# Optimization experiments

Measured on AMD Instinct MI355X. Metric: run time of the kernel, lower is better.

## Reference

```python
import jax, jax.numpy as jnp
import numpy as np

N, M, E = 400000, 100000, 3200000
C_FEAT = 61            # per-point feature channels
D_IN = 64              # 3 (rel xyz) + C_FEAT
D0, D1, D2 = 64, 128, 256  # mlp = [64, 128, 256]
EPS = 1e-5


def setup_inputs() -> dict:
    key = jax.random.key(0)
    ks = jax.random.split(key, 16)
    inp = {}
    inp['point_bxyz'] = jax.random.uniform(ks[0], (N, 4), dtype=jnp.float32) * 50.0
    inp['point_feat'] = jax.random.normal(ks[1], (N, C_FEAT), dtype=jnp.float32)
    inp['sample_idx'] = jax.random.randint(ks[2], (M,), 0, N)
    inp['e_point'] = jax.random.randint(ks[3], (E,), 0, N)
    inp['e_new'] = jnp.sort(jax.random.randint(ks[4], (E,), 0, M))
    # PointConv: Linear(D_IN -> D0)
    inp['W0'] = jax.random.normal(ks[5], (D_IN, D0), dtype=jnp.float32) / np.sqrt(D_IN)
    inp['b0'] = jnp.zeros((D0,), dtype=jnp.float32)
    # mlp_convs[0]: Linear(D0 -> D1) + BN
    inp['W1'] = jax.random.normal(ks[6], (D0, D1), dtype=jnp.float32) / np.sqrt(D0)
    inp['b1'] = jnp.zeros((D1,), dtype=jnp.float32)
    inp['g1'] = jnp.ones((D1,), dtype=jnp.float32)
    inp['beta1'] = jnp.zeros((D1,), dtype=jnp.float32)
    # mlp_convs[1]: Linear(D1 -> D2) + BN
    inp['W2'] = jax.random.normal(ks[7], (D1, D2), dtype=jnp.float32) / np.sqrt(D1)
    inp['b2'] = jnp.zeros((D2,), dtype=jnp.float32)
    inp['g2'] = jnp.ones((D2,), dtype=jnp.float32)
    inp['beta2'] = jnp.zeros((D2,), dtype=jnp.float32)
    return inp


def _bn_relu(x, g, b):
    # BatchNorm1d in training mode: batch stats, biased variance
    mu = x.mean(axis=0)
    var = x.var(axis=0)
    return jax.nn.relu((x - mu) * jax.lax.rsqrt(var + EPS) * g + b)


def reference(point_bxyz, point_feat, sample_idx, e_point, e_new,
              W0, b0, W1, b1, g1, beta1, W2, b2, g2, beta2):
    num_new = sample_idx.shape[0]
    new_bxyz = point_bxyz[sample_idx]                      # [M, 4]
    # PointConv: per-edge relative position encoding + feature gather
    rel = point_bxyz[e_point, 1:4] - new_bxyz[e_new, 1:4]  # [E, 3]
    edge_in = jnp.concatenate([rel, point_feat[e_point]], axis=-1)  # [E, D_IN]
    h = jax.nn.relu(edge_in @ W0 + b0)                     # [E, D0]
    # per-neighborhood max aggregation (scatter-max), empty segments -> 0
    agg = jax.ops.segment_max(h, e_new, num_segments=num_new)
    agg = jnp.where(jnp.isneginf(agg), 0.0, agg)           # [M, D0]
    # trailing Linear + BN + ReLU stack
    x = _bn_relu(agg @ W1 + b1, g1, beta1)                 # [M, D1]
    x = _bn_relu(x @ W2 + b2, g2, beta2)                   # [M, D2]
    return new_bxyz, x
```

## Files before the change

### kernel.cpp

```cpp
#include <hip/hip_runtime.h>

#define EPS 1e-5f
#define ECHUNK 64

typedef _Float16 half8 __attribute__((ext_vector_type(8)));
typedef _Float16 half4v __attribute__((ext_vector_type(4)));
typedef float float4v __attribute__((ext_vector_type(4)));

static __device__ __forceinline__ unsigned pkmax16(unsigned a, unsigned b) {
    unsigned d;
    asm("v_pk_max_f16 %0, %1, %2" : "=v"(d) : "v"(a), "v"(b));
    return d;
}

__global__ void gather_kernel(const float4* __restrict__ bxyz, const int* __restrict__ sidx,
                              float4* __restrict__ out, int M) {
    int i = blockIdx.x * blockDim.x + threadIdx.x;
    if (i < M) out[i] = bxyz[sidx[i]];
}

__global__ void prep_kernel(const float* __restrict__ W0, const float* __restrict__ W1,
                            const float* __restrict__ W2, _Float16* __restrict__ W0t,
                            _Float16* __restrict__ W1t, _Float16* __restrict__ W2t) {
    int i = blockIdx.x * blockDim.x + threadIdx.x;
    if (i < 4096) {
        int k = i >> 6, n = i & 63;
        W0t[(size_t)n * 64 + k] = (_Float16)W0[i];
    } else if (i < 12288) {
        int j = i - 4096; int k = j >> 7, n = j & 127;
        W1t[(size_t)n * 64 + k] = (_Float16)W1[j];
    } else if (i < 45056) {
        int j = i - 12288; int k = j >> 8, n = j & 255;
        W2t[(size_t)n * 128 + k] = (_Float16)W2[j];
    }
}

__global__ __launch_bounds__(256, 4) void point_kernel(
    const float* __restrict__ feat, const float4* __restrict__ bxyz4,
    const _Float16* __restrict__ W0t, const float* __restrict__ b0,
    _Float16* __restrict__ GDh, int N) {
    __shared__ _Float16 As[128 * 72];
    int t = threadIdx.x;
    int row0 = blockIdx.x * 128;
    if (t < 128) {
        int r = min(row0 + t, N - 1);
        float4 P = bxyz4[r];
        As[t * 72 + 0] = (_Float16)P.y;
        As[t * 72 + 1] = (_Float16)P.z;
        As[t * 72 + 2] = (_Float16)P.w;
    }
    const float* fbase = feat + (size_t)row0 * 61;
    int avail = (int)min((size_t)7808, (size_t)(N - row0) * 61);
#pragma unroll
    for (int j = 0; j < 8; ++j) {
        int base = (t + j * 256) * 4;
        if (base < avail) {
            float4 v = *(const float4*)&fbase[base];
            float fv[4] = {v.x, v.y, v.z, v.w};
#pragma unroll
            for (int u = 0; u < 4; ++u) {
                int flat = base + u;
                int r = flat / 61;
                int k = flat - r * 61;
                As[r * 72 + 3 + k] = (_Float16)fv[u];
            }
        }
    }
    __syncthreads();
    int w = t >> 6, lane = t & 63, quad = lane >> 4, l16 = lane & 15;
    int mwave = w * 32;
    float4v acc[2][4] = {};
#pragma unroll
    for (int kc = 0; kc < 2; ++kc) {
        int koff = kc * 32 + quad * 8;
        half8 af[2], bf[4];
#pragma unroll
        for (int mt = 0; mt < 2; ++mt)
            af[mt] = *(const half8*)&As[(mwave + mt * 16 + l16) * 72 + koff];
#pragma unroll
        for (int nt = 0; nt < 4; ++nt)
            bf[nt] = *(const half8*)&W0t[(size_t)(nt * 16 + l16) * 64 + koff];
#pragma unroll
        for (int mt = 0; mt < 2; ++mt)
#pragma unroll
            for (int nt = 0; nt < 4; ++nt)
                acc[mt][nt] = __builtin_amdgcn_mfma_f32_16x16x32_f16(af[mt], bf[nt], acc[mt][nt], 0, 0, 0);
    }
    float b0v[4];
#pragma unroll
    for (int nt = 0; nt < 4; ++nt) b0v[nt] = b0[nt * 16 + l16];
    __syncthreads();
#pragma unroll
    for (int mt = 0; mt < 2; ++mt)
#pragma unroll
        for (int i = 0; i < 4; ++i) {
            int rloc = mwave + mt * 16 + quad * 4 + i;
#pragma unroll
            for (int nt = 0; nt < 4; ++nt)
                As[rloc * 72 + nt * 16 + l16] = (_Float16)(acc[mt][nt][i] + b0v[nt]);
        }
    __syncthreads();
#pragma unroll
    for (int j = 0; j < 4; ++j) {
        int i8 = t + j * 256;
        int r = i8 >> 3, c8 = i8 & 7;
        if (row0 + r < N)
            *(half8*)&GDh[(size_t)(row0 + r) * 64 + c8 * 8] = *(const half8*)&As[r * 72 + c8 * 8];
    }
}

__global__ __launch_bounds__(256, 8) void edge_kernel(
    const float4* __restrict__ nbxyz4,
    const int* __restrict__ e_point, const int* __restrict__ e_new,
    const _Float16* __restrict__ GDh, const float* __restrict__ W0,
    float* __restrict__ agg, int E) {
    int lane = threadIdx.x & 63;
    int gwave = blockIdx.x * 4 + (threadIdx.x >> 6);
    int base = __builtin_amdgcn_readfirstlane(gwave * ECHUNK);
    if (base >= E) return;
    int n = min(ECHUNK, E - base);

    if (n == ECHUNK) {
        bool hi = lane >= 32;
        int c0 = lane & 31;
        int ch = c0 * 2 + (hi ? 1 : 0);
        float wx = W0[ch], wy = W0[64 + ch], wz = W0[128 + ch];
        const unsigned NEGP = 0xFBFFFBFFu;

        int ep = e_point[base + lane];
        int en = e_new[base + lane];

        int prev = __shfl_up(en, 1);
        unsigned long long bm = __ballot(lane == 0 || en != prev);
        unsigned blo = __builtin_amdgcn_readfirstlane((unsigned)bm);
        unsigned bhi = __builtin_amdgcn_readfirstlane((unsigned)(bm >> 32));
        unsigned long long bmask = (((unsigned long long)bhi << 32) | blo) & ~1ull;

        int curseg = __builtin_amdgcn_readlane(en, 0);
        unsigned amax = NEGP;
        int laneoff = c0 * 4;
        int permbase = hi ? 4 : 0;

#define FLUSH_SEG()  do {                                                          \
        unsigned other_ = (unsigned)__shfl_xor((int)amax, 32);                     \
        unsigned comb_ = pkmax16(amax, other_);                                    \
        unsigned bits_ = hi ? (comb_ >> 16) : (comb_ & 0xffffu);                   \
        _Float16 hm_ = __builtin_bit_cast(_Float16, (unsigned short)bits_);        \
        float4 Q_ = nbxyz4[curseg];                                                \
        float S_ = fmaf(Q_.y, wx, fmaf(Q_.z, wy, Q_.w * wz));                      \
        float v_ = fmaxf(0.f, (float)hm_ - S_);                                    \
        atomicMax((int*)&agg[(size_t)curseg * 64 + ch], __float_as_int(v_));       \
    } while (0)

#pragma unroll
        for (int grp = 0; grp < 2; ++grp) {
            unsigned gu[16];
#pragma unroll
            for (int j = 0; j < 16; ++j) {
                int p = __builtin_amdgcn_ds_bpermute(permbase + (grp * 16 + j) * 8, ep);
                unsigned off = ((unsigned)p << 7) + laneoff;
                gu[j] = *(const unsigned*)((const char*)GDh + off);
            }
#pragma unroll
            for (int j = 0; j < 16; ++j) {
                int e0 = (grp * 16 + j) * 2;
                if ((bmask >> e0) & 1) {
                    FLUSH_SEG();
                    curseg = __builtin_amdgcn_readlane(en, e0);
                    amax = NEGP;
                }
                if ((bmask >> (e0 + 1)) & 1) {
                    amax = pkmax16(amax, hi ? NEGP : gu[j]);
                    FLUSH_SEG();
                    curseg = __builtin_amdgcn_readlane(en, e0 + 1);
                    amax = hi ? gu[j] : NEGP;
                } else {
                    amax = pkmax16(amax, gu[j]);
                }
            }
        }
        FLUSH_SEG();
#undef FLUSH_SEG
    } else {
        float wx = W0[lane], wy = W0[64 + lane], wz = W0[128 + lane];
        int idx = min(base + lane, E - 1);
        int ep = e_point[idx];
        int en = e_new[idx];
        int curseg = -1;
        float runmax = 0.f, S = 0.f;
        for (int e = 0; e < n; ++e) {
            int p = __builtin_amdgcn_readlane(ep, e);
            int s = __builtin_amdgcn_readlane(en, e);
            if (s != curseg) {
                if (curseg >= 0)
                    atomicMax((int*)&agg[(size_t)curseg * 64 + lane], __float_as_int(runmax));
                curseg = s;
                runmax = 0.f;
                float4 Q = nbxyz4[s];
                S = fmaf(Q.y, wx, fmaf(Q.z, wy, Q.w * wz));
            }
            float h = (float)GDh[(size_t)p * 64 + lane] - S;
            runmax = fmaxf(runmax, h);
        }
        if (curseg >= 0)
            atomicMax((int*)&agg[(size_t)curseg * 64 + lane], __float_as_int(runmax));
    }
}

__global__ __launch_bounds__(256, 2) void gemm1_kernel(
    const float* __restrict__ agg, const _Float16* __restrict__ W1t,
    _Float16* __restrict__ y1h, float* __restrict__ p1sum, float* __restrict__ p1sq, int M) {
    __shared__ _Float16 As[128 * 72];
    __shared__ float red[4096];
    int t = threadIdx.x;
    int row0 = blockIdx.x * 128;
#pragma unroll
    for (int j = 0; j < 8; ++j) {
        int i4 = t + j * 256;
        int r = i4 >> 4, k4 = i4 & 15;
        float4 v = make_float4(0.f, 0.f, 0.f, 0.f);
        if (row0 + r < M) v = ((const float4*)agg)[(size_t)(row0 + r) * 16 + k4];
        half4v h;
        h[0] = (_Float16)v.x; h[1] = (_Float16)v.y; h[2] = (_Float16)v.z; h[3] = (_Float16)v.w;
        *(half4v*)&As[r * 72 + k4 * 4] = h;
    }
    __syncthreads();
    int w = t >> 6, lane = t & 63, quad = lane >> 4, l16 = lane & 15;
    int mwave = w * 32;
    float4v acc[2][8] = {};
#pragma unroll
    for (int kc = 0; kc < 2; ++kc) {
        int koff = kc * 32 + quad * 8;
        half8 af[2], bf[8];
#pragma unroll
        for (int mt = 0; mt < 2; ++mt)
            af[mt] = *(const half8*)&As[(mwave + mt * 16 + l16) * 72 + koff];
#pragma unroll
        for (int nt = 0; nt < 8; ++nt)
            bf[nt] = *(const half8*)&W1t[(size_t)(nt * 16 + l16) * 64 + koff];
#pragma unroll
        for (int mt = 0; mt < 2; ++mt)
#pragma unroll
            for (int nt = 0; nt < 8; ++nt)
                acc[mt][nt] = __builtin_amdgcn_mfma_f32_16x16x32_f16(af[mt], bf[nt], acc[mt][nt], 0, 0, 0);
    }
    float s[8] = {}, q[8] = {};
#pragma unroll
    for (int mt = 0; mt < 2; ++mt)
#pragma unroll
        for (int i = 0; i < 4; ++i)
#pragma unroll
            for (int nt = 0; nt < 8; ++nt) {
                float a = acc[mt][nt][i];
                s[nt] += a; q[nt] += a * a;
            }
    int slot = w * 4 + quad;
#pragma unroll
    for (int nt = 0; nt < 8; ++nt) {
        int c = nt * 16 + l16;
        red[c * 16 + slot] = s[nt];
        red[2048 + c * 16 + slot] = q[nt];
    }
    __syncthreads();
    if (t < 128) {
        float ss = 0.f, qq = 0.f;
#pragma unroll
        for (int i = 0; i < 16; ++i) { ss += red[t * 16 + i]; qq += red[2048 + t * 16 + i]; }
        p1sum[(size_t)blockIdx.x * 128 + t] = ss;
        p1sq[(size_t)blockIdx.x * 128 + t] = qq;
    }
#pragma unroll
    for (int half = 0; half < 2; ++half) {
#pragma unroll
        for (int mt = 0; mt < 2; ++mt)
#pragma unroll
            for (int i = 0; i < 4; ++i) {
                int rloc = mwave + mt * 16 + quad * 4 + i;
#pragma unroll
                for (int nt = 0; nt < 4; ++nt)
                    As[rloc * 72 + nt * 16 + l16] = (_Float16)acc[mt][half * 4 + nt][i];
            }
        __syncthreads();
#pragma unroll
        for (int j = 0; j < 4; ++j) {
            int i8 = t + j * 256;
            int r = i8 >> 3, c8 = i8 & 7;
            if (row0 + r < M)
                *(half8*)&y1h[(size_t)(row0 + r) * 128 + half * 64 + c8 * 8] =
                    *(const half8*)&As[r * 72 + c8 * 8];
        }
        __syncthreads();
    }
}

__global__ void stats_kernel(const float* __restrict__ psum, const float* __restrict__ psq,
                             const float* __restrict__ g, const float* __restrict__ beta,
                             float* __restrict__ scale, float* __restrict__ shift,
                             int nblk, int ncols, float invM) {
    __shared__ float ss[256], qq[256];
    int c = blockIdx.x;
    int t = threadIdx.x;
    float s = 0.f, q = 0.f;
    for (int b = t; b < nblk; b += 256) {
        s += psum[(size_t)b * ncols + c];
        q += psq[(size_t)b * ncols + c];
    }
    ss[t] = s; qq[t] = q;
    __syncthreads();
    for (int off = 128; off > 0; off >>= 1) {
        if (t < off) { ss[t] += ss[t + off]; qq[t] += qq[t + off]; }
        __syncthreads();
    }
    if (t == 0) {
        float mean = ss[0] * invM;
        float var = qq[0] * invM - mean * mean;
        float sc = g[c] * rsqrtf(var + EPS);
        scale[c] = sc;
        shift[c] = beta[c] - mean * sc;
    }
}

__global__ __launch_bounds__(256, 2) void gemm2_kernel(
    const _Float16* __restrict__ y1h, const _Float16* __restrict__ W2t,
    const float* __restrict__ scale1, const float* __restrict__ shift1,
    float* __restrict__ yout, float* __restrict__ p2sum, float* __restrict__ p2sq,
    int M, int nbn) {
    __shared__ _Float16 As[128 * 136];
    __shared__ _Float16 Bs[128 * 136];
    int t = threadIdx.x;
    int bm = blockIdx.x / nbn;
    int bn = blockIdx.x % nbn;
    int row0 = bm * 128;
#pragma unroll
    for (int j = 0; j < 8; ++j) {
        int i8 = t + j * 256;
        int r = i8 >> 4, k8 = i8 & 15;
        half8 hv = {};
        if (row0 + r < M) {
            half8 y = *(const half8*)&y1h[(size_t)(row0 + r) * 128 + k8 * 8];
            float4 sca = ((const float4*)scale1)[k8 * 2];
            float4 scb = ((const float4*)scale1)[k8 * 2 + 1];
            float4 sha = ((const float4*)shift1)[k8 * 2];
            float4 shb = ((const float4*)shift1)[k8 * 2 + 1];
            float sc[8] = {sca.x, sca.y, sca.z, sca.w, scb.x, scb.y, scb.z, scb.w};
            float sh[8] = {sha.x, sha.y, sha.z, sha.w, shb.x, shb.y, shb.z, shb.w};
#pragma unroll
            for (int u = 0; u < 8; ++u)
                hv[u] = (_Float16)fmaxf(0.f, fmaf((float)y[u], sc[u], sh[u]));
        }
        *(half8*)&As[r * 136 + k8 * 8] = hv;
    }
    int n0 = bn * 128;
#pragma unroll
    for (int j = 0; j < 8; ++j) {
        int i8 = t + j * 256;
        int nn = i8 >> 4, k8 = i8 & 15;
        *(half8*)&Bs[nn * 136 + k8 * 8] = *(const half8*)&W2t[(size_t)(n0 + nn) * 128 + k8 * 8];
    }
    __syncthreads();
    int w = t >> 6, lane = t & 63;
    int quad = lane >> 4, l16 = lane & 15;
    int mwave = (w >> 1) * 64, nwave = (w & 1) * 64;
    float4v acc[4][4] = {};
#pragma unroll
    for (int kc = 0; kc < 4; ++kc) {
        int koff = kc * 32 + quad * 8;
        half8 af[4], bf[4];
#pragma unroll
        for (int mt = 0; mt < 4; ++mt)
            af[mt] = *(const half8*)&As[(mwave + mt * 16 + l16) * 136 + koff];
#pragma unroll
        for (int nt = 0; nt < 4; ++nt)
            bf[nt] = *(const half8*)&Bs[(nwave + nt * 16 + l16) * 136 + koff];
#pragma unroll
        for (int mt = 0; mt < 4; ++mt)
#pragma unroll
            for (int nt = 0; nt < 4; ++nt)
                acc[mt][nt] = __builtin_amdgcn_mfma_f32_16x16x32_f16(af[mt], bf[nt], acc[mt][nt], 0, 0, 0);
    }
    float s[4] = {}, q[4] = {};
    int colbase = n0 + nwave + l16;
#pragma unroll
    for (int mt = 0; mt < 4; ++mt) {
#pragma unroll
        for (int i = 0; i < 4; ++i) {
            int row = row0 + mwave + mt * 16 + quad * 4 + i;
            if (row < M) {
#pragma unroll
                for (int nt = 0; nt < 4; ++nt)
                    yout[(size_t)row * 256 + colbase + nt * 16] = acc[mt][nt][i];
            }
#pragma unroll
            for (int nt = 0; nt < 4; ++nt) {
                float a = acc[mt][nt][i];
                s[nt] += a; q[nt] += a * a;
            }
        }
    }
    __syncthreads();
    float* red = (float*)As;
    int slot = (w >> 1) * 4 + quad;
#pragma unroll
    for (int nt = 0; nt < 4; ++nt) {
        int c = (w & 1) * 64 + nt * 16 + l16;
        red[c * 8 + slot] = s[nt];
        red[1024 + c * 8 + slot] = q[nt];
    }
    __syncthreads();
    if (t < 128) {
        float ss = 0.f, qq = 0.f;
#pragma unroll
        for (int i = 0; i < 8; ++i) { ss += red[t * 8 + i]; qq += red[1024 + t * 8 + i]; }
        p2sum[(size_t)bm * 256 + n0 + t] = ss;
        p2sq[(size_t)bm * 256 + n0 + t] = qq;
    }
}

__global__ void apply2_kernel(float4* __restrict__ x, const float* __restrict__ scale2,
                              const float* __restrict__ shift2, int n4) {
    int i = blockIdx.x * blockDim.x + threadIdx.x;
    if (i >= n4) return;
    int c4 = i & 63;
    float4 v = x[i];
    float4 sc = ((const float4*)scale2)[c4];
    float4 sh = ((const float4*)shift2)[c4];
    v.x = fmaxf(0.f, fmaf(v.x, sc.x, sh.x));
    v.y = fmaxf(0.f, fmaf(v.y, sc.y, sh.y));
    v.z = fmaxf(0.f, fmaf(v.z, sc.z, sh.z));
    v.w = fmaxf(0.f, fmaf(v.w, sc.w, sh.w));
    x[i] = v;
}

extern "C" void kernel_launch(void* const* d_in, const int* in_sizes, int n_in,
                              void* d_out, int out_size, void* d_ws, size_t ws_size,
                              hipStream_t stream) {
    const float* bxyz  = (const float*)d_in[0];
    const float* feat  = (const float*)d_in[1];
    const int*   sidx  = (const int*)d_in[2];
    const int*   e_point = (const int*)d_in[3];
    const int*   e_new = (const int*)d_in[4];
    const float* W0    = (const float*)d_in[5];
    const float* b0    = (const float*)d_in[6];
    const float* W1    = (const float*)d_in[7];
    const float* g1    = (const float*)d_in[9];
    const float* beta1 = (const float*)d_in[10];
    const float* W2    = (const float*)d_in[11];
    const float* g2    = (const float*)d_in[13];
    const float* beta2 = (const float*)d_in[14];
    int N = in_sizes[0] / 4;
    int M = in_sizes[2];
    int E = in_sizes[3];

    float* out0 = (float*)d_out;
    float* out1 = (float*)d_out + (size_t)M * 4;

    float* ws = (float*)d_ws;
    size_t o = 0;
    float* agg = ws + o; o += (size_t)M * 64;
    _Float16* y1h = (_Float16*)(ws + o); o += (size_t)M * 64;
    _Float16* GDh = (_Float16*)(ws + o); o += (size_t)N * 32;
    _Float16* W0t = (_Float16*)(ws + o); o += 2048;
    _Float16* W1t = (_Float16*)(ws + o); o += 4096;
    _Float16* W2t = (_Float16*)(ws + o); o += 16384;
    int nblk1 = (M + 127) / 128;
    int nblk2m = (M + 127) / 128;
    int nbn = 2;
    float* p1sum = ws + o; o += (size_t)nblk1 * 128;
    float* p1sq  = ws + o; o += (size_t)nblk1 * 128;
    float* p2sum = ws + o; o += (size_t)nblk2m * 256;
    float* p2sq  = ws + o; o += (size_t)nblk2m * 256;
    float* scale1 = ws + o; o += 128;
    float* shift1 = ws + o; o += 128;
    float* scale2 = ws + o; o += 256;
    float* shift2 = ws + o; o += 256;

    hipMemsetAsync(agg, 0, (size_t)M * 64 * sizeof(float), stream);
    gather_kernel<<<(M + 255) / 256, 256, 0, stream>>>((const float4*)bxyz, sidx, (float4*)out0, M);
    prep_kernel<<<176, 256, 0, stream>>>(W0, W1, W2, W0t, W1t, W2t);
    point_kernel<<<(N + 127) / 128, 256, 0, stream>>>(feat, (const float4*)bxyz, W0t, b0, GDh, N);
    int nwaves = (E + ECHUNK - 1) / ECHUNK;
    edge_kernel<<<(nwaves + 3) / 4, 256, 0, stream>>>((const float4*)out0, e_point, e_new,
                                                      GDh, W0, agg, E);
    gemm1_kernel<<<nblk1, 256, 0, stream>>>(agg, W1t, y1h, p1sum, p1sq, M);
    stats_kernel<<<128, 256, 0, stream>>>(p1sum, p1sq, g1, beta1, scale1, shift1, nblk1, 128, 1.f / M);
    gemm2_kernel<<<nblk2m * nbn, 256, 0, stream>>>(y1h, W2t, scale1, shift1, out1, p2sum, p2sq, M, nbn);
    stats_kernel<<<256, 256, 0, stream>>>(p2sum, p2sq, g2, beta2, scale2, shift2, nblk2m, 256, 1.f / M);
    apply2_kernel<<<((M * 64) + 255) / 256, 256, 0, stream>>>((float4*)out1, scale2, shift2, M * 64);
}
```

Baseline: 389.0 us.

## Stage GEMM2 output in fp16 and precompute fp16 point input matrix

GEMM2 now writes its pre-BN output as fp16 to a workspace buffer (reusing the GDh region) through a shared-memory staged, coalesced store. The final BN+ReLU pass reads that fp16 buffer and writes fp32 output, replacing the fp32 write-then-read-modify-write on the output. The point input matrix (xyz plus features) is converted to fp16 once in a merged prep/gather kernel that also replaces two small launches, so point_kernel loads aligned half8 rows instead of doing unaligned repacking. The cost is an extra write and read of the fp16 point matrix and fp16 rounding of pre-BN activations.

Result: no change. 387.4 us (-0.4%).

```diff
diff --git a/kernel.cpp b/kernel.cpp
--- a/kernel.cpp
+++ b/kernel.cpp
@@ -13,15 +13,13 @@
     return d;
 }
 
-__global__ void gather_kernel(const float4* __restrict__ bxyz, const int* __restrict__ sidx,
-                              float4* __restrict__ out, int M) {
-    int i = blockIdx.x * blockDim.x + threadIdx.x;
-    if (i < M) out[i] = bxyz[sidx[i]];
-}
-
-__global__ void prep_kernel(const float* __restrict__ W0, const float* __restrict__ W1,
-                            const float* __restrict__ W2, _Float16* __restrict__ W0t,
-                            _Float16* __restrict__ W1t, _Float16* __restrict__ W2t) {
+__global__ void prep_gather_kernel(const float* __restrict__ W0, const float* __restrict__ W1,
+                                   const float* __restrict__ W2, _Float16* __restrict__ W0t,
+                                   _Float16* __restrict__ W1t, _Float16* __restrict__ W2t,
+                                   const float4* __restrict__ bxyz, const int* __restrict__ sidx,
+                                   float4* __restrict__ out, int M,
+                                   const float* __restrict__ feat, _Float16* __restrict__ Pmat,
+                                   int N) {
     int i = blockIdx.x * blockDim.x + threadIdx.x;
     if (i < 4096) {
         int k = i >> 6, n = i & 63;
@@ -32,39 +30,45 @@
     } else if (i < 45056) {
         int j = i - 12288; int k = j >> 8, n = j & 255;
         W2t[(size_t)n * 128 + k] = (_Float16)W2[j];
+    } else if (i < 45056 + M) {
+        int j = i - 45056;
+        out[j] = bxyz[sidx[j]];
+    } else {
+        int j2 = i - (45056 + M);
+        if (j2 < N * 8) {
+            int r = j2 >> 3, c8 = j2 & 7;
+            const float* frow = feat + (size_t)r * 61;
+            half8 h;
+            if (c8 == 0) {
+                float4 P = bxyz[r];
+                h[0] = (_Float16)P.y;
+                h[1] = (_Float16)P.z;
+                h[2] = (_Float16)P.w;
+#pragma unroll
+                for (int u = 0; u < 5; ++u) h[3 + u] = (_Float16)frow[u];
+            } else {
+                const float* p = frow + c8 * 8 - 3;
+#pragma unroll
+                for (int u = 0; u < 8; ++u) h[u] = (_Float16)p[u];
+            }
+            *(half8*)&Pmat[(size_t)r * 64 + c8 * 8] = h;
+        }
     }
 }
 
 __global__ __launch_bounds__(256, 4) void point_kernel(
-    const float* __restrict__ feat, const float4* __restrict__ bxyz4,
+    const _Float16* __restrict__ Pmat,
     const _Float16* __restrict__ W0t, const float* __restrict__ b0,
     _Float16* __restrict__ GDh, int N) {
     __shared__ _Float16 As[128 * 72];
     int t = threadIdx.x;
     int row0 = blockIdx.x * 128;
-    if (t < 128) {
-        int r = min(row0 + t, N - 1);
-        float4 P = bxyz4[r];
-        As[t * 72 + 0] = (_Float16)P.y;
-        As[t * 72 + 1] = (_Float16)P.z;
-        As[t * 72 + 2] = (_Float16)P.w;
-    }
-    const float* fbase = feat + (size_t)row0 * 61;
-    int avail = (int)min((size_t)7808, (size_t)(N - row0) * 61);
-#pragma unroll
-    for (int j = 0; j < 8; ++j) {
-        int base = (t + j * 256) * 4;
-        if (base < avail) {
-            float4 v = *(const float4*)&fbase[base];
-            float fv[4] = {v.x, v.y, v.z, v.w};
-#pragma unroll
-            for (int u = 0; u < 4; ++u) {
-                int flat = base + u;
-                int r = flat / 61;
-                int k = flat - r * 61;
-                As[r * 72 + 3 + k] = (_Float16)fv[u];
-            }
-        }
+#pragma unroll
+    for (int j = 0; j < 4; ++j) {
+        int i8 = t + j * 256;
+        int r = i8 >> 3, c8 = i8 & 7;
+        int rr = min(row0 + r, N - 1);
+        *(half8*)&As[r * 72 + c8 * 8] = *(const half8*)&Pmat[(size_t)rr * 64 + c8 * 8];
     }
     __syncthreads();
     int w = t >> 6, lane = t & 63, quad = lane >> 4, l16 = lane & 15;
@@ -323,7 +327,7 @@
 __global__ __launch_bounds__(256, 2) void gemm2_kernel(
     const _Float16* __restrict__ y1h, const _Float16* __restrict__ W2t,
     const float* __restrict__ scale1, const float* __restrict__ shift1,
-    float* __restrict__ yout, float* __restrict__ p2sum, float* __restrict__ p2sq,
+    _Float16* __restrict__ y2h, float* __restrict__ p2sum, float* __restrict__ p2sq,
     int M, int nbn) {
     __shared__ _Float16 As[128 * 136];
     __shared__ _Float16 Bs[128 * 136];
@@ -379,26 +383,17 @@
                 acc[mt][nt] = __builtin_amdgcn_mfma_f32_16x16x32_f16(af[mt], bf[nt], acc[mt][nt], 0, 0, 0);
     }
     float s[4] = {}, q[4] = {};
-    int colbase = n0 + nwave + l16;
-#pragma unroll
-    for (int mt = 0; mt < 4; ++mt) {
-#pragma unroll
-        for (int i = 0; i < 4; ++i) {
-            int row = row0 + mwave + mt * 16 + quad * 4 + i;
-            if (row < M) {
-#pragma unroll
-                for (int nt = 0; nt < 4; ++nt)
-                    yout[(size_t)row * 256 + colbase + nt * 16] = acc[mt][nt][i];
-            }
+#pragma unroll
+    for (int mt = 0; mt < 4; ++mt)
+#pragma unroll
+        for (int i = 0; i < 4; ++i)
 #pragma unroll
             for (int nt = 0; nt < 4; ++nt) {
                 float a = acc[mt][nt][i];
                 s[nt] += a; q[nt] += a * a;
             }
-        }
-    }
-    __syncthreads();
-    float* red = (float*)As;
+    __syncthreads();
+    float* red = (float*)Bs;
     int slot = (w >> 1) * 4 + quad;
 #pragma unroll
     for (int nt = 0; nt < 4; ++nt) {
@@ -406,6 +401,15 @@
         red[c * 8 + slot] = s[nt];
         red[1024 + c * 8 + slot] = q[nt];
     }
+#pragma unroll
+    for (int mt = 0; mt < 4; ++mt)
+#pragma unroll
+        for (int i = 0; i < 4; ++i) {
+            int rloc = mwave + mt * 16 + quad * 4 + i;
+#pragma unroll
+            for (int nt = 0; nt < 4; ++nt)
+                As[rloc * 136 + nwave + nt * 16 + l16] = (_Float16)acc[mt][nt][i];
+        }
     __syncthreads();
     if (t < 128) {
         float ss = 0.f, qq = 0.f;
@@ -414,21 +418,38 @@
         p2sum[(size_t)bm * 256 + n0 + t] = ss;
         p2sq[(size_t)bm * 256 + n0 + t] = qq;
     }
-}
-
-__global__ void apply2_kernel(float4* __restrict__ x, const float* __restrict__ scale2,
-                              const float* __restrict__ shift2, int n4) {
+#pragma unroll
+    for (int j = 0; j < 8; ++j) {
+        int i8 = t + j * 256;
+        int r = i8 >> 4, c8 = i8 & 15;
+        if (row0 + r < M)
+            *(half8*)&y2h[(size_t)(row0 + r) * 256 + n0 + c8 * 8] =
+                *(const half8*)&As[r * 136 + c8 * 8];
+    }
+}
+
+__global__ void apply2_kernel(const _Float16* __restrict__ y2h, float4* __restrict__ x,
+                              const float* __restrict__ scale2, const float* __restrict__ shift2,
+                              int n8) {
     int i = blockIdx.x * blockDim.x + threadIdx.x;
-    if (i >= n4) return;
-    int c4 = i & 63;
-    float4 v = x[i];
-    float4 sc = ((const float4*)scale2)[c4];
-    float4 sh = ((const float4*)shift2)[c4];
-    v.x = fmaxf(0.f, fmaf(v.x, sc.x, sh.x));
-    v.y = fmaxf(0.f, fmaf(v.y, sc.y, sh.y));
-    v.z = fmaxf(0.f, fmaf(v.z, sc.z, sh.z));
-    v.w = fmaxf(0.f, fmaf(v.w, sc.w, sh.w));
-    x[i] = v;
+    if (i >= n8) return;
+    int c8 = i & 31;
+    half8 y = *(const half8*)&y2h[(size_t)i * 8];
+    float4 sc0 = ((const float4*)scale2)[c8 * 2];
+    float4 sc1 = ((const float4*)scale2)[c8 * 2 + 1];
+    float4 sh0 = ((const float4*)shift2)[c8 * 2];
+    float4 sh1 = ((const float4*)shift2)[c8 * 2 + 1];
+    float4 a, b;
+    a.x = fmaxf(0.f, fmaf((float)y[0], sc0.x, sh0.x));
+    a.y = fmaxf(0.f, fmaf((float)y[1], sc0.y, sh0.y));
+    a.z = fmaxf(0.f, fmaf((float)y[2], sc0.z, sh0.z));
+    a.w = fmaxf(0.f, fmaf((float)y[3], sc0.w, sh0.w));
+    b.x = fmaxf(0.f, fmaf((float)y[4], sc1.x, sh1.x));
+    b.y = fmaxf(0.f, fmaf((float)y[5], sc1.y, sh1.y));
+    b.z = fmaxf(0.f, fmaf((float)y[6], sc1.z, sh1.z));
+    b.w = fmaxf(0.f, fmaf((float)y[7], sc1.w, sh1.w));
+    x[(size_t)i * 2] = a;
+    x[(size_t)i * 2 + 1] = b;
 }
 
 extern "C" void kernel_launch(void* const* d_in, const int* in_sizes, int n_in,
@@ -473,17 +494,21 @@
     float* shift1 = ws + o; o += 128;
     float* scale2 = ws + o; o += 256;
     float* shift2 = ws + o; o += 256;
-
+    _Float16* Pmat = (_Float16*)ws;
+    _Float16* y2h = GDh;
+
+    int total_t = 45056 + M + N * 8;
+    prep_gather_kernel<<<(total_t + 255) / 256, 256, 0, stream>>>(
+        W0, W1, W2, W0t, W1t, W2t, (const float4*)bxyz, sidx, (float4*)out0, M,
+        feat, Pmat, N);
+    point_kernel<<<(N + 127) / 128, 256, 0, stream>>>(Pmat, W0t, b0, GDh, N);
     hipMemsetAsync(agg, 0, (size_t)M * 64 * sizeof(float), stream);
-    gather_kernel<<<(M + 255) / 256, 256, 0, stream>>>((const float4*)bxyz, sidx, (float4*)out0, M);
-    prep_kernel<<<176, 256, 0, stream>>>(W0, W1, W2, W0t, W1t, W2t);
-    point_kernel<<<(N + 127) / 128, 256, 0, stream>>>(feat, (const float4*)bxyz, W0t, b0, GDh, N);
     int nwaves = (E + ECHUNK - 1) / ECHUNK;
     edge_kernel<<<(nwaves + 3) / 4, 256, 0, stream>>>((const float4*)out0, e_point, e_new,
                                                       GDh, W0, agg, E);
     gemm1_kernel<<<nblk1, 256, 0, stream>>>(agg, W1t, y1h, p1sum, p1sq, M);
     stats_kernel<<<128, 256, 0, stream>>>(p1sum, p1sq, g1, beta1, scale1, shift1, nblk1, 128, 1.f / M);
-    gemm2_kernel<<<nblk2m * nbn, 256, 0, stream>>>(y1h, W2t, scale1, shift1, out1, p2sum, p2sq, M, nbn);
+    gemm2_kernel<<<nblk2m * nbn, 256, 0, stream>>>(y1h, W2t, scale1, shift1, y2h, p2sum, p2sq, M, nbn);
     stats_kernel<<<256, 256, 0, stream>>>(p2sum, p2sq, g2, beta2, scale2, shift2, nblk2m, 256, 1.f / M);
-    apply2_kernel<<<((M * 64) + 255) / 256, 256, 0, stream>>>((float4*)out1, scale2, shift2, M * 64);
-}
+    apply2_kernel<<<((M * 32) + 255) / 256, 256, 0, stream>>>(y2h, (float4*)out1, scale2, shift2, M * 32);
+}
```

## Recompute second GEMM instead of storing pre-BN output, fuse prep/gather/memset

Applied to the files above, without the earlier changes.

The second GEMM now runs twice. The first pass only computes the per-column sum and sum-of-squares partials and writes no output. The second pass recomputes the GEMM, applies the BN2 scale/shift and ReLU in registers, and writes the final output through shared memory with coalesced float4 stores. This removes the full-size fp32 write, read and rewrite of the [M,256] intermediate that the separate apply kernel needed, at the cost of repeating the small K=128 GEMM. The weight prep, sample gather and agg zeroing are also merged into one launch, replacing a memset and two kernels.

New measurement: 383.8 us. Within noise of the previous version (-1.3%).

```diff
diff --git a/kernel.cpp b/kernel.cpp
--- a/kernel.cpp
+++ b/kernel.cpp
@@ -13,15 +13,11 @@
     return d;
 }
 
-__global__ void gather_kernel(const float4* __restrict__ bxyz, const int* __restrict__ sidx,
-                              float4* __restrict__ out, int M) {
-    int i = blockIdx.x * blockDim.x + threadIdx.x;
-    if (i < M) out[i] = bxyz[sidx[i]];
-}
-
-__global__ void prep_kernel(const float* __restrict__ W0, const float* __restrict__ W1,
-                            const float* __restrict__ W2, _Float16* __restrict__ W0t,
-                            _Float16* __restrict__ W1t, _Float16* __restrict__ W2t) {
+__global__ void prep_gather_kernel(const float* __restrict__ W0, const float* __restrict__ W1,
+                                   const float* __restrict__ W2, _Float16* __restrict__ W0t,
+                                   _Float16* __restrict__ W1t, _Float16* __restrict__ W2t,
+                                   const float4* __restrict__ bxyz, const int* __restrict__ sidx,
+                                   float4* __restrict__ out, int M, float4* __restrict__ agg4) {
     int i = blockIdx.x * blockDim.x + threadIdx.x;
     if (i < 4096) {
         int k = i >> 6, n = i & 63;
@@ -32,6 +28,12 @@
     } else if (i < 45056) {
         int j = i - 12288; int k = j >> 8, n = j & 255;
         W2t[(size_t)n * 128 + k] = (_Float16)W2[j];
+    } else if (i < 45056 + M) {
+        int j = i - 45056;
+        out[j] = bxyz[sidx[j]];
+    } else {
+        int j = i - (45056 + M);
+        if (j < M * 16) agg4[j] = make_float4(0.f, 0.f, 0.f, 0.f);
     }
 }
 
@@ -320,11 +322,10 @@
     }
 }
 
-__global__ __launch_bounds__(256, 2) void gemm2_kernel(
+__global__ __launch_bounds__(256, 2) void gemm2s_kernel(
     const _Float16* __restrict__ y1h, const _Float16* __restrict__ W2t,
     const float* __restrict__ scale1, const float* __restrict__ shift1,
-    float* __restrict__ yout, float* __restrict__ p2sum, float* __restrict__ p2sq,
-    int M, int nbn) {
+    float* __restrict__ p2sum, float* __restrict__ p2sq, int M, int nbn) {
     __shared__ _Float16 As[128 * 136];
     __shared__ _Float16 Bs[128 * 136];
     int t = threadIdx.x;
@@ -379,26 +380,17 @@
                 acc[mt][nt] = __builtin_amdgcn_mfma_f32_16x16x32_f16(af[mt], bf[nt], acc[mt][nt], 0, 0, 0);
     }
     float s[4] = {}, q[4] = {};
-    int colbase = n0 + nwave + l16;
-#pragma unroll
-    for (int mt = 0; mt < 4; ++mt) {
-#pragma unroll
-        for (int i = 0; i < 4; ++i) {
-            int row = row0 + mwave + mt * 16 + quad * 4 + i;
-            if (row < M) {
-#pragma unroll
-                for (int nt = 0; nt < 4; ++nt)
-                    yout[(size_t)row * 256 + colbase + nt * 16] = acc[mt][nt][i];
-            }
+#pragma unroll
+    for (int mt = 0; mt < 4; ++mt)
+#pragma unroll
+        for (int i = 0; i < 4; ++i)
 #pragma unroll
             for (int nt = 0; nt < 4; ++nt) {
                 float a = acc[mt][nt][i];
                 s[nt] += a; q[nt] += a * a;
             }
-        }
-    }
-    __syncthreads();
-    float* red = (float*)As;
+    __syncthreads();
+    float* red = (float*)Bs;
     int slot = (w >> 1) * 4 + quad;
 #pragma unroll
     for (int nt = 0; nt < 4; ++nt) {
@@ -416,19 +408,98 @@
     }
 }
 
-__global__ void apply2_kernel(float4* __restrict__ x, const float* __restrict__ scale2,
-                              const float* __restrict__ shift2, int n4) {
-    int i = blockIdx.x * blockDim.x + threadIdx.x;
-    if (i >= n4) return;
-    int c4 = i & 63;
-    float4 v = x[i];
-    float4 sc = ((const float4*)scale2)[c4];
-    float4 sh = ((const float4*)shift2)[c4];
-    v.x = fmaxf(0.f, fmaf(v.x, sc.x, sh.x));
-    v.y = fmaxf(0.f, fmaf(v.y, sc.y, sh.y));
-    v.z = fmaxf(0.f, fmaf(v.z, sc.z, sh.z));
-    v.w = fmaxf(0.f, fmaf(v.w, sc.w, sh.w));
-    x[i] = v;
+__global__ __launch_bounds__(256, 2) void gemm2a_kernel(
+    const _Float16* __restrict__ y1h, const _Float16* __restrict__ W2t,
+    const float* __restrict__ scale1, const float* __restrict__ shift1,
+    const float* __restrict__ scale2, const float* __restrict__ shift2,
+    float* __restrict__ out1, int M, int nbn) {
+    __shared__ _Float16 As[128 * 136];
+    __shared__ _Float16 Bs[128 * 136];
+    int t = threadIdx.x;
+    int bm = blockIdx.x / nbn;
+    int bn = blockIdx.x % nbn;
+    int row0 = bm * 128;
+#pragma unroll
+    for (int j = 0; j < 8; ++j) {
+        int i8 = t + j * 256;
+        int r = i8 >> 4, k8 = i8 & 15;
+        half8 hv = {};
+        if (row0 + r < M) {
+            half8 y = *(const half8*)&y1h[(size_t)(row0 + r) * 128 + k8 * 8];
+            float4 sca = ((const float4*)scale1)[k8 * 2];
+            float4 scb = ((const float4*)scale1)[k8 * 2 + 1];
+            float4 sha = ((const float4*)shift1)[k8 * 2];
+            float4 shb = ((const float4*)shift1)[k8 * 2 + 1];
+            float sc[8] = {sca.x, sca.y, sca.z, sca.w, scb.x, scb.y, scb.z, scb.w};
+            float sh[8] = {sha.x, sha.y, sha.z, sha.w, shb.x, shb.y, shb.z, shb.w};
+#pragma unroll
+            for (int u = 0; u < 8; ++u)
+                hv[u] = (_Float16)fmaxf(0.f, fmaf((float)y[u], sc[u], sh[u]));
+        }
+        *(half8*)&As[r * 136 + k8 * 8] = hv;
+    }
+    int n0 = bn * 128;
+#pragma unroll
+    for (int j = 0; j < 8; ++j) {
+        int i8 = t + j * 256;
+        int nn = i8 >> 4, k8 = i8 & 15;
+        *(half8*)&Bs[nn * 136 + k8 * 8] = *(const half8*)&W2t[(size_t)(n0 + nn) * 128 + k8 * 8];
+    }
+    __syncthreads();
+    int w = t >> 6, lane = t & 63;
+    int quad = lane >> 4, l16 = lane & 15;
+    int mwave = (w >> 1) * 64, nwave = (w & 1) * 64;
+    float4v acc[4][4] = {};
+#pragma unroll
+    for (int kc = 0; kc < 4; ++kc) {
+        int koff = kc * 32 + quad * 8;
+        half8 af[4], bf[4];
+#pragma unroll
+        for (int mt = 0; mt < 4; ++mt)
+            af[mt] = *(const half8*)&As[(mwave + mt * 16 + l16) * 136 + koff];
+#pragma unroll
+        for (int nt = 0; nt < 4; ++nt)
+            bf[nt] = *(const half8*)&Bs[(nwave + nt * 16 + l16) * 136 + koff];
+#pragma unroll
+        for (int mt = 0; mt < 4; ++mt)
+#pragma unroll
+            for (int nt = 0; nt < 4; ++nt)
+                acc[mt][nt] = __builtin_amdgcn_mfma_f32_16x16x32_f16(af[mt], bf[nt], acc[mt][nt], 0, 0, 0);
+    }
+    float sc2[4], sh2[4];
+#pragma unroll
+    for (int nt = 0; nt < 4; ++nt) {
+        int c = n0 + nwave + nt * 16 + l16;
+        sc2[nt] = scale2[c];
+        sh2[nt] = shift2[c];
+    }
+    __syncthreads();
+    float* As32 = (float*)As;
+#pragma unroll
+    for (int half = 0; half < 2; ++half) {
+        if ((w & 1) == half) {
+#pragma unroll
+            for (int mt = 0; mt < 4; ++mt)
+#pragma unroll
+                for (int i = 0; i < 4; ++i) {
+                    int rloc = mwave + mt * 16 + quad * 4 + i;
+#pragma unroll
+                    for (int nt = 0; nt < 4; ++nt)
+                        As32[rloc * 68 + nt * 16 + l16] =
+                            fmaxf(0.f, fmaf(acc[mt][nt][i], sc2[nt], sh2[nt]));
+                }
+        }
+        __syncthreads();
+#pragma unroll
+        for (int j = 0; j < 8; ++j) {
+            int i4 = t + j * 256;
+            int r = i4 >> 4, c4 = i4 & 15;
+            if (row0 + r < M)
+                *(float4*)&out1[(size_t)(row0 + r) * 256 + n0 + half * 64 + c4 * 4] =
+                    *(const float4*)&As32[r * 68 + c4 * 4];
+        }
+        __syncthreads();
+    }
 }
 
 extern "C" void kernel_launch(void* const* d_in, const int* in_sizes, int n_in,
@@ -474,16 +545,17 @@
     float* scale2 = ws + o; o += 256;
     float* shift2 = ws + o; o += 256;
 
-    hipMemsetAsync(agg, 0, (size_t)M * 64 * sizeof(float), stream);
-    gather_kernel<<<(M + 255) / 256, 256, 0, stream>>>((const float4*)bxyz, sidx, (float4*)out0, M);
-    prep_kernel<<<176, 256, 0, stream>>>(W0, W1, W2, W0t, W1t, W2t);
+    int total_t = 45056 + M + M * 16;
+    prep_gather_kernel<<<(total_t + 255) / 256, 256, 0, stream>>>(
+        W0, W1, W2, W0t, W1t, W2t, (const float4*)bxyz, sidx, (float4*)out0, M, (float4*)agg);
     point_kernel<<<(N + 127) / 128, 256, 0, stream>>>(feat, (const float4*)bxyz, W0t, b0, GDh, N);
     int nwaves = (E + ECHUNK - 1) / ECHUNK;
     edge_kernel<<<(nwaves + 3) / 4, 256, 0, stream>>>((const float4*)out0, e_point, e_new,
                                                       GDh, W0, agg, E);
     gemm1_kernel<<<nblk1, 256, 0, stream>>>(agg, W1t, y1h, p1sum, p1sq, M);
     stats_kernel<<<128, 256, 0, stream>>>(p1sum, p1sq, g1, beta1, scale1, shift1, nblk1, 128, 1.f / M);
-    gemm2_kernel<<<nblk2m * nbn, 256, 0, stream>>>(y1h, W2t, scale1, shift1, out1, p2sum, p2sq, M, nbn);
+    gemm2s_kernel<<<nblk2m * nbn, 256, 0, stream>>>(y1h, W2t, scale1, shift1, p2sum, p2sq, M, nbn);
     stats_kernel<<<256, 256, 0, stream>>>(p2sum, p2sq, g2, beta2, scale2, shift2, nblk2m, 256, 1.f / M);
-    apply2_kernel<<<((M * 64) + 255) / 256, 256, 0, stream>>>((float4*)out1, scale2, shift2, M * 64);
-}
+    gemm2a_kernel<<<nblk2m * nbn, 256, 0, stream>>>(y1h, W2t, scale1, shift1, scale2, shift2,
+                                                    out1, M, nbn);
+}
```
